# Kernel optimization log

Hardware: AMD Instinct MI355X
Metric: run time of the kernel (lower is better)

The kernel has to match this reference:

```python
import jax, jax.numpy as jnp
import numpy as np

B, S, E, H, L, FF = 32, 256, 768, 12, 2, 2048
DH = E // H
N_HIST, N_TGT = 128, 127  # fixed layout: pos0=type0, 1..128=type1 (hist), 129..255=type2 (target)
HIST_MASK_RATIO, MASK_RATIO, TAU = 0.5, 0.5, 1.0
KEEP_HIST = max(1, int(N_HIST * (1.0 - HIST_MASK_RATIO)))  # 64
KEEP_TGT = max(1, int(N_TGT * (1.0 - MASK_RATIO)))        # 63
INFERENCE = False
EPS = 1e-5
NEG = -1e30


def _sinusoidal_pe():
    pos = np.arange(257, dtype=np.float32)[:, None]
    div = np.exp(np.arange(0, E, 2, dtype=np.float32) * (-np.log(10000.0) / E))
    pe = np.zeros((257, E), np.float32)
    pe[:, 0::2] = np.sin(pos * div)
    pe[:, 1::2] = np.cos(pos * div)
    return jnp.asarray(pe)


def setup_inputs() -> dict:
    key = jax.random.key(0)
    ks = jax.random.split(key, 12)
    rn = lambda k, sh, s=1.0: jax.random.normal(k, sh, dtype=jnp.float32) * s
    inp = {}
    inp['token_embeds'] = rn(ks[0], (B, S, E))
    inp['attention_mask'] = jnp.zeros((B, S), dtype=bool)  # no padding
    inp['position_ids'] = jnp.tile(jnp.arange(S, dtype=jnp.int32), (B, 1))
    row = jnp.concatenate([jnp.zeros((1,), jnp.int32), jnp.ones((N_HIST,), jnp.int32), jnp.full((N_TGT,), 2, jnp.int32)])
    inp['type_ids'] = jnp.tile(row, (B, 1))
    inp['gumbel_hist'] = jax.random.gumbel(ks[1], (B, S), dtype=jnp.float32)
    inp['gumbel_target'] = jax.random.gumbel(ks[2], (B, S), dtype=jnp.float32)
    inp['pe'] = _sinusoidal_pe()
    inp['type_emb'] = rn(ks[3], (3, E), 0.02)
    inp['ln_w'] = jnp.ones((E,), jnp.float32); inp['ln_b'] = jnp.zeros((E,), jnp.float32)
    inp['dense_w'] = rn(ks[4], (E, E), 0.02); inp['dense_b'] = jnp.zeros((E,), jnp.float32)
    inp['qkv_w'] = rn(ks[5], (L, 3 * E, E), 0.02); inp['qkv_b'] = jnp.zeros((L, 3 * E), jnp.float32)
    inp['out_w'] = rn(ks[6], (L, E, E), 0.02); inp['out_b'] = jnp.zeros((L, E), jnp.float32)
    inp['ln1_w'] = jnp.ones((L, E), jnp.float32); inp['ln1_b'] = jnp.zeros((L, E), jnp.float32)
    inp['lin1_w'] = rn(ks[7], (L, FF, E), 0.02); inp['lin1_b'] = jnp.zeros((L, FF), jnp.float32)
    inp['lin2_w'] = rn(ks[8], (L, E, FF), 0.02); inp['lin2_b'] = jnp.zeros((L, E), jnp.float32)
    inp['ln2_w'] = jnp.ones((L, E), jnp.float32); inp['ln2_b'] = jnp.zeros((L, E), jnp.float32)
    return inp


def _ln(x, w, b):
    m = x.mean(-1, keepdims=True)
    v = jnp.mean((x - m) ** 2, -1, keepdims=True)
    return (x - m) * jax.lax.rsqrt(v + EPS) * w + b


def _masked_softmax(score, m):
    e = jnp.exp(score) * m
    return e / jnp.sum(e, -1, keepdims=True)


def _gumbel_topk(prob, valid, gumbel, keep_num):
    vm = valid.astype(prob.dtype)
    logits = jnp.where(valid, jnp.log(jnp.where(valid, prob, 1.0)), NEG)
    gl = jnp.where(valid, (logits + gumbel) / TAU, NEG)
    y_soft = jax.nn.softmax(gl, axis=-1)  # invalid positions get exactly 0
    idx = jax.lax.top_k(y_soft, keep_num)[1]
    y_hard = jnp.zeros_like(y_soft).at[jnp.arange(B)[:, None], idx].set(1.0)
    return (y_hard - jax.lax.stop_gradient(y_soft) + y_soft) * vm


def reference(token_embeds, attention_mask, position_ids, type_ids, gumbel_hist, gumbel_target,
              pe, type_emb, ln_w, ln_b, dense_w, dense_b, qkv_w, qkv_b, out_w, out_b,
              ln1_w, ln1_b, lin1_w, lin1_b, lin2_w, lin2_b, ln2_w, ln2_b):
    # get_input_embeds (dropout = identity in eval)
    x = _ln(token_embeds + pe[position_ids] + type_emb[type_ids], ln_w, ln_b)
    # TransformerEncoder (post-norm, relu FFN, key_padding_mask)
    kpm = attention_mask[:, None, None, :]
    for l in range(L):
        qkv = x @ qkv_w[l].T + qkv_b[l]
        q, k, v = jnp.split(qkv, 3, axis=-1)
        q = q.reshape(B, S, H, DH); k = k.reshape(B, S, H, DH); v = v.reshape(B, S, H, DH)
        sc = jnp.einsum('bqhd,bkhd->bhqk', q, k) / np.float32(np.sqrt(DH))
        sc = jnp.where(kpm, NEG, sc)
        o = jnp.einsum('bhqk,bkhd->bqhd', jax.nn.softmax(sc, -1), v).reshape(B, S, E)
        x = _ln(x + o @ out_w[l].T + out_b[l], ln1_w[l], ln1_b[l])
        f = jax.nn.relu(x @ lin1_w[l].T + lin1_b[l]) @ lin2_w[l].T + lin2_b[l]
        x = _ln(x + f, ln2_w[l], ln2_b[l])
    out = _ln(x, ln_w, ln_b)
    out = jnp.tanh(out @ dense_w.T + dense_b)
    # cosine similarity (torch eps=1e-8)
    na = jnp.linalg.norm(token_embeds, axis=-1)
    nb = jnp.linalg.norm(out, axis=-1)
    cos = jnp.sum(token_embeds * out, -1) / jnp.maximum(na * nb, 1e-8)
    hist_mask = type_ids == 1
    tgt_mask = type_ids == 2
    hp = _masked_softmax(cos, hist_mask.astype(cos.dtype))
    tp0 = _masked_softmax(cos, tgt_mask.astype(cos.dtype))
    tp = tp0 if INFERENCE else 1.0 - tp0
    hist_ret = _gumbel_topk(hp, hist_mask, gumbel_hist, KEEP_HIST)
    tgt_ret = _gumbel_topk(tp, tgt_mask, gumbel_target, KEEP_TGT)
    return hist_ret + tgt_ret
```

## Files before the change

kernel.cpp:

```cpp
#include <hip/hip_runtime.h>
#include <math.h>

#define B_ 32
#define S_ 256
#define E_ 768
#define H_ 12
#define L_ 2
#define FF_ 2048
#define NEGV -1e30f

typedef __attribute__((ext_vector_type(8))) short bf16x8;
typedef __attribute__((ext_vector_type(4))) float f32x4;

__device__ __forceinline__ short bf16_rne(float x) {
  unsigned u = __float_as_uint(x);
  u += 0x7fffu + ((u >> 16) & 1u);
  return (short)(u >> 16);
}
__device__ __forceinline__ float bf16_to_f32(short h) {
  return __uint_as_float(((unsigned)(unsigned short)h) << 16);
}
__device__ __forceinline__ void split_bf16(float v, short& h, short& l) {
  h = bf16_rne(v);
  l = bf16_rne(v - bf16_to_f32(h));
}

__device__ __forceinline__ void gl2lds16(const short* g, short* s) {
  __builtin_amdgcn_global_load_lds((const __attribute__((address_space(1))) void*)g,
                                   (__attribute__((address_space(3))) void*)s, 16, 0, 0);
}

__device__ __forceinline__ float block_sum256(float v) {
  __shared__ float sh[4];
  int lane = threadIdx.x & 63, w = threadIdx.x >> 6;
#pragma unroll
  for (int off = 32; off; off >>= 1) v += __shfl_down(v, off);
  if (lane == 0) sh[w] = v;
  __syncthreads();
  float tot = sh[0] + sh[1] + sh[2] + sh[3];
  __syncthreads();
  return tot;
}

__global__ __launch_bounds__(256) void embed_ln_kernel(
    const float* __restrict__ tok, const int* __restrict__ pos,
    const int* __restrict__ typ, const float* __restrict__ pe,
    const float* __restrict__ temb, const float* __restrict__ w,
    const float* __restrict__ b, float* __restrict__ out,
    short* __restrict__ ohi, short* __restrict__ olo) {
  int row = blockIdx.x;
  int t = threadIdx.x;
  int p = pos[row], ty = typ[row];
  const float* tr = tok + (size_t)row * E_;
  const float* pr = pe + (size_t)p * E_;
  const float* yr = temb + (size_t)ty * E_;
  float v0 = tr[t] + pr[t] + yr[t];
  float v1 = tr[t + 256] + pr[t + 256] + yr[t + 256];
  float v2 = tr[t + 512] + pr[t + 512] + yr[t + 512];
  float m = block_sum256(v0 + v1 + v2) * (1.f / E_);
  float d0 = v0 - m, d1 = v1 - m, d2 = v2 - m;
  float var = block_sum256(d0 * d0 + d1 * d1 + d2 * d2) * (1.f / E_);
  float rs = 1.f / sqrtf(var + 1e-5f);
  size_t base = (size_t)row * E_;
  float r0 = d0 * rs * w[t] + b[t];
  float r1 = d1 * rs * w[t + 256] + b[t + 256];
  float r2 = d2 * rs * w[t + 512] + b[t + 512];
  out[base + t] = r0; out[base + t + 256] = r1; out[base + t + 512] = r2;
  short h, l;
  split_bf16(r0, h, l); ohi[base + t] = h; olo[base + t] = l;
  split_bf16(r1, h, l); ohi[base + t + 256] = h; olo[base + t + 256] = l;
  split_bf16(r2, h, l); ohi[base + t + 512] = h; olo[base + t + 512] = l;
}

__global__ __launch_bounds__(256) void ln_kernel(
    const float* __restrict__ in, const float* __restrict__ w,
    const float* __restrict__ b, float* __restrict__ out,
    short* __restrict__ ohi, short* __restrict__ olo) {
  int row = blockIdx.x;
  int t = threadIdx.x;
  const float* p = in + (size_t)row * E_;
  float v0 = p[t], v1 = p[t + 256], v2 = p[t + 512];
  float m = block_sum256(v0 + v1 + v2) * (1.f / E_);
  float d0 = v0 - m, d1 = v1 - m, d2 = v2 - m;
  float var = block_sum256(d0 * d0 + d1 * d1 + d2 * d2) * (1.f / E_);
  float rs = 1.f / sqrtf(var + 1e-5f);
  size_t base = (size_t)row * E_;
  float r0 = d0 * rs * w[t] + b[t];
  float r1 = d1 * rs * w[t + 256] + b[t + 256];
  float r2 = d2 * rs * w[t + 512] + b[t + 512];
  if (out) {
    out[base + t] = r0; out[base + t + 256] = r1; out[base + t + 512] = r2;
  }
  short h, l;
  split_bf16(r0, h, l); ohi[base + t] = h; olo[base + t] = l;
  split_bf16(r1, h, l); ohi[base + t + 256] = h; olo[base + t + 256] = l;
  split_bf16(r2, h, l); ohi[base + t + 512] = h; olo[base + t + 512] = l;
}

__global__ __launch_bounds__(256) void split_kernel(
    const float* __restrict__ src, short* __restrict__ hi,
    short* __restrict__ lo, int n4) {
  int i = blockIdx.x * 256 + threadIdx.x;
  if (i >= n4) return;
  float4 v = ((const float4*)src)[i];
  short4 h, l;
  split_bf16(v.x, h.x, l.x);
  split_bf16(v.y, h.y, l.y);
  split_bf16(v.z, h.z, l.z);
  split_bf16(v.w, h.w, l.w);
  ((short4*)hi)[i] = h;
  ((short4*)lo)[i] = l;
}

template <int ACT, int RES, int OSPLIT>
__global__ __launch_bounds__(256, 2) void gemm_dp(
    const short* __restrict__ Ahi, const short* __restrict__ Alo,
    const short* __restrict__ Whi, const short* __restrict__ Wlo,
    const float* __restrict__ bias, const float* __restrict__ Rres,
    float* __restrict__ Cf, short* __restrict__ Chi, short* __restrict__ Clo,
    int M, int N, int K, int nx, int cpx) {
  __shared__ short lds[2 * 16384];
  const int t = threadIdx.x;
  const int l = t & 63;
  const int w = t >> 6;
  int id = blockIdx.x;
  int id2 = (id & 7) * cpx + (id >> 3);
  const int n0 = (id2 % nx) * 128, m0 = (id2 / nx) * 128;
  const int wm = (w >> 1) * 64, wn = (w & 1) * 64;

  const int g_kb = (l & 3) ^ ((l >> 3) & 3);
  const int r0 = w * 16 + (l >> 2);
  const int r1 = r0 + 64;
  const size_t aof0 = (size_t)(m0 + r0) * K + g_kb * 8;
  const size_t aof1 = (size_t)(m0 + r1) * K + g_kb * 8;
  const size_t wof0 = (size_t)(n0 + r0) * K + g_kb * 8;
  const size_t wof1 = (size_t)(n0 + r1) * K + g_kb * 8;
  const short* pAh0 = Ahi + aof0; const short* pAh1 = Ahi + aof1;
  const short* pAl0 = Alo + aof0; const short* pAl1 = Alo + aof1;
  const short* pWh0 = Whi + wof0; const short* pWh1 = Whi + wof1;
  const short* pWl0 = Wlo + wof0; const short* pWl1 = Wlo + wof1;

  const int kb_r = ((l >> 4) ^ ((l >> 1) & 3)) * 8;
  const short* ra = lds + (wm + (l & 15)) * 32 + kb_r;
  const short* rb = lds + (wn + (l & 15)) * 32 + kb_r;

  f32x4 acc[4][4] = {};
  const int ns = K >> 5;

  auto stage = [&](int buf, int k0) {
    short* base = lds + buf * 16384;
    gl2lds16(pAh0 + k0, base + w * 512);
    gl2lds16(pAh1 + k0, base + (4 + w) * 512);
    gl2lds16(pAl0 + k0, base + 4096 + w * 512);
    gl2lds16(pAl1 + k0, base + 4096 + (4 + w) * 512);
    gl2lds16(pWh0 + k0, base + 8192 + w * 512);
    gl2lds16(pWh1 + k0, base + 8192 + (4 + w) * 512);
    gl2lds16(pWl0 + k0, base + 12288 + w * 512);
    gl2lds16(pWl1 + k0, base + 12288 + (4 + w) * 512);
  };

  stage(0, 0);

  for (int s = 0; s < ns; ++s) {
    const int bp = s & 1;
    __builtin_amdgcn_s_barrier();
    if (s + 1 < ns) {
      stage(bp ^ 1, (s + 1) * 32);
      __builtin_amdgcn_sched_barrier(0);
      asm volatile("s_waitcnt vmcnt(8)" ::: "memory");
    } else {
      __builtin_amdgcn_sched_barrier(0);
      asm volatile("s_waitcnt vmcnt(0)" ::: "memory");
    }
    __builtin_amdgcn_s_barrier();

    const short* rab = ra + bp * 16384;
    const short* rbb = rb + bp * 16384;
    bf16x8 ah[4], al[4], bh[4], bl[4];
#pragma unroll
    for (int i = 0; i < 4; i++) {
      ah[i] = *(const bf16x8*)(rab + i * 512);
      al[i] = *(const bf16x8*)(rab + 4096 + i * 512);
      bh[i] = *(const bf16x8*)(rbb + 8192 + i * 512);
      bl[i] = *(const bf16x8*)(rbb + 12288 + i * 512);
    }
    __builtin_amdgcn_s_setprio(1);
#pragma unroll
    for (int mi = 0; mi < 4; mi++)
#pragma unroll
      for (int ni = 0; ni < 4; ni++) {
        acc[mi][ni] = __builtin_amdgcn_mfma_f32_16x16x32_bf16(ah[mi], bh[ni], acc[mi][ni], 0, 0, 0);
        acc[mi][ni] = __builtin_amdgcn_mfma_f32_16x16x32_bf16(ah[mi], bl[ni], acc[mi][ni], 0, 0, 0);
        acc[mi][ni] = __builtin_amdgcn_mfma_f32_16x16x32_bf16(al[mi], bh[ni], acc[mi][ni], 0, 0, 0);
      }
    __builtin_amdgcn_s_setprio(0);
  }

  const int col_l = l & 15;
  const int row_l = (l >> 4) * 4;
#pragma unroll
  for (int mi = 0; mi < 4; mi++) {
#pragma unroll
    for (int ni = 0; ni < 4; ni++) {
      int col = n0 + wn + ni * 16 + col_l;
      float bv = bias[col];
#pragma unroll
      for (int r = 0; r < 4; r++) {
        int row = m0 + wm + mi * 16 + row_l + r;
        float v = acc[mi][ni][r] + bv;
        if (RES) v += Rres[(size_t)row * N + col];
        if (ACT == 1) v = fmaxf(v, 0.f);
        if (ACT == 2) v = tanhf(v);
        if (OSPLIT) {
          short h2, l2;
          split_bf16(v, h2, l2);
          Chi[(size_t)row * N + col] = h2;
          Clo[(size_t)row * N + col] = l2;
        } else {
          Cf[(size_t)row * N + col] = v;
        }
      }
    }
  }
}

template <int ACT, int RES>
__global__ __launch_bounds__(256, 2) void gemm_dp2(
    const short* __restrict__ Ahi, const short* __restrict__ Alo,
    const short* __restrict__ Whi, const short* __restrict__ Wlo,
    const float* __restrict__ bias, const float* __restrict__ Rres,
    float* __restrict__ Cf, int M, int N, int K, int nx, int cpx) {
  __shared__ short lds[2 * 20480];
  const int t = threadIdx.x;
  const int l = t & 63;
  const int w = t >> 6;
  int id = blockIdx.x;
  int id2 = (id & 7) * cpx + (id >> 3);
  const int n0 = (id2 % nx) * 192, m0 = (id2 / nx) * 128;
  const int wm = (w >> 1) * 64;
  const int wn = (w & 1) * 96;

  const int g_kb = (l & 3) ^ ((l >> 3) & 3);
  const int srow = w * 16 + (l >> 2);
  const size_t a0 = (size_t)(m0 + srow) * K + g_kb * 8;
  const size_t a1 = (size_t)(m0 + 64 + srow) * K + g_kb * 8;
  const size_t w0 = (size_t)(n0 + srow) * K + g_kb * 8;
  const size_t w1 = (size_t)(n0 + 64 + srow) * K + g_kb * 8;
  const size_t w2 = (size_t)(n0 + 128 + srow) * K + g_kb * 8;
  const short* pAh0 = Ahi + a0; const short* pAh1 = Ahi + a1;
  const short* pAl0 = Alo + a0; const short* pAl1 = Alo + a1;
  const short* pWh0 = Whi + w0; const short* pWh1 = Whi + w1; const short* pWh2 = Whi + w2;
  const short* pWl0 = Wlo + w0; const short* pWl1 = Wlo + w1; const short* pWl2 = Wlo + w2;

  const int kb_r = ((l >> 4) ^ ((l >> 1) & 3)) * 8;
  const short* ra = lds + (wm + (l & 15)) * 32 + kb_r;
  const short* rb = lds + 8192 + (wn + (l & 15)) * 32 + kb_r;

  f32x4 acc[4][6] = {};
  const int ns = K >> 5;

  auto stage = [&](int buf, int k0) {
    short* base = lds + buf * 20480;
    gl2lds16(pAh0 + k0, base + w * 512);
    gl2lds16(pAh1 + k0, base + 2048 + w * 512);
    gl2lds16(pAl0 + k0, base + 4096 + w * 512);
    gl2lds16(pAl1 + k0, base + 4096 + 2048 + w * 512);
    gl2lds16(pWh0 + k0, base + 8192 + w * 512);
    gl2lds16(pWh1 + k0, base + 8192 + 2048 + w * 512);
    gl2lds16(pWh2 + k0, base + 8192 + 4096 + w * 512);
    gl2lds16(pWl0 + k0, base + 14336 + w * 512);
    gl2lds16(pWl1 + k0, base + 14336 + 2048 + w * 512);
    gl2lds16(pWl2 + k0, base + 14336 + 4096 + w * 512);
  };

  stage(0, 0);

  for (int s = 0; s < ns; ++s) {
    const int bp = s & 1;
    __builtin_amdgcn_s_barrier();
    if (s + 1 < ns) {
      stage(bp ^ 1, (s + 1) * 32);
      __builtin_amdgcn_sched_barrier(0);
      asm volatile("s_waitcnt vmcnt(10)" ::: "memory");
    } else {
      __builtin_amdgcn_sched_barrier(0);
      asm volatile("s_waitcnt vmcnt(0)" ::: "memory");
    }
    __builtin_amdgcn_s_barrier();

    const short* rab = ra + bp * 20480;
    const short* rbb = rb + bp * 20480;
    bf16x8 bh[6], bl[6];
#pragma unroll
    for (int i = 0; i < 6; i++) {
      bh[i] = *(const bf16x8*)(rbb + i * 512);
      bl[i] = *(const bf16x8*)(rbb + 6144 + i * 512);
    }
    __builtin_amdgcn_s_setprio(1);
#pragma unroll
    for (int mi = 0; mi < 4; mi++) {
      bf16x8 ah = *(const bf16x8*)(rab + mi * 512);
      bf16x8 al = *(const bf16x8*)(rab + 4096 + mi * 512);
#pragma unroll
      for (int ni = 0; ni < 6; ni++) {
        acc[mi][ni] = __builtin_amdgcn_mfma_f32_16x16x32_bf16(ah, bh[ni], acc[mi][ni], 0, 0, 0);
        acc[mi][ni] = __builtin_amdgcn_mfma_f32_16x16x32_bf16(ah, bl[ni], acc[mi][ni], 0, 0, 0);
        acc[mi][ni] = __builtin_amdgcn_mfma_f32_16x16x32_bf16(al, bh[ni], acc[mi][ni], 0, 0, 0);
      }
    }
    __builtin_amdgcn_s_setprio(0);
  }

  const int col_l = l & 15;
  const int row_l = (l >> 4) * 4;
#pragma unroll
  for (int mi = 0; mi < 4; mi++) {
#pragma unroll
    for (int ni = 0; ni < 6; ni++) {
      int col = n0 + wn + ni * 16 + col_l;
      float bv = bias[col];
#pragma unroll
      for (int r = 0; r < 4; r++) {
        int row = m0 + wm + mi * 16 + row_l + r;
        float v = acc[mi][ni][r] + bv;
        if (RES) v += Rres[(size_t)row * N + col];
        if (ACT == 2) v = tanhf(v);
        Cf[(size_t)row * N + col] = v;
      }
    }
  }
}

__global__ __launch_bounds__(256, 2) void attn_kernel(
    const float* __restrict__ qkv, short* __restrict__ t1h,
    short* __restrict__ t1l) {
  __shared__ short lds[16384];
  const int qt = blockIdx.x, h = blockIdx.y, b = blockIdx.z;
  const int t = threadIdx.x;
  const int w = t >> 6, l = t & 63;
  const int li = l & 15, lh = l >> 4;

  short* kh = lds;
  short* kl = lds + 4096;
  short* ph = lds + 8192 + w * 2048;
  short* pl = ph + 1024;

  const int tok0 = b * S_ + qt * 64;

  bf16x8 qh[2], ql[2];
  {
    const float* qrow = qkv + (size_t)(tok0 + w * 16 + li) * 2304 + h * 64 + lh * 8;
#pragma unroll
    for (int s = 0; s < 2; s++) {
      float4 f0 = *(const float4*)(qrow + s * 32);
      float4 f1 = *(const float4*)(qrow + s * 32 + 4);
      float f[8] = {f0.x, f0.y, f0.z, f0.w, f1.x, f1.y, f1.z, f1.w};
      bf16x8 hv, lv;
#pragma unroll
      for (int j = 0; j < 8; j++) {
        short hs, ls2;
        split_bf16(f[j], hs, ls2);
        hv[j] = hs; lv[j] = ls2;
      }
      qh[s] = hv; ql[s] = lv;
    }
  }

  const int skk = t >> 2, sd0 = (t & 3) * 16;

  f32x4 acc[16] = {};

  const float* kbase = qkv + (size_t)(b * S_) * 2304 + 768 + h * 64;
#pragma unroll
  for (int c = 0; c < 4; c++) {
    __syncthreads();
    {
      const float* src = kbase + (size_t)(c * 64 + skk) * 2304 + sd0;
#pragma unroll
      for (int i = 0; i < 4; i++) {
        float4 f = *(const float4*)(src + i * 4);
        int d = sd0 + i * 4;
        short4 hv, lv;
        split_bf16(f.x, hv.x, lv.x);
        split_bf16(f.y, hv.y, lv.y);
        split_bf16(f.z, hv.z, lv.z);
        split_bf16(f.w, hv.w, lv.w);
        int off = skk * 64 + ((((d >> 3) ^ (skk & 7)) & 7) << 3) + (d & 7);
        *(short4*)(kh + off) = hv;
        *(short4*)(kl + off) = lv;
      }
    }
    __syncthreads();
#pragma unroll
    for (int nn = 0; nn < 4; nn++) {
      const int krow = nn * 16 + li;
#pragma unroll
      for (int s = 0; s < 2; s++) {
        const int off = krow * 64 + ((((s * 4 + lh) ^ (li & 7)) & 7) << 3);
        bf16x8 bh = *(const bf16x8*)(kh + off);
        bf16x8 bl = *(const bf16x8*)(kl + off);
        acc[c * 4 + nn] = __builtin_amdgcn_mfma_f32_16x16x32_bf16(qh[s], bh, acc[c * 4 + nn], 0, 0, 0);
        acc[c * 4 + nn] = __builtin_amdgcn_mfma_f32_16x16x32_bf16(qh[s], bl, acc[c * 4 + nn], 0, 0, 0);
        acc[c * 4 + nn] = __builtin_amdgcn_mfma_f32_16x16x32_bf16(ql[s], bh, acc[c * 4 + nn], 0, 0, 0);
      }
    }
  }

  float rs_[4];
#pragma unroll
  for (int r = 0; r < 4; r++) {
    float m = -3.4e38f;
#pragma unroll
    for (int fi = 0; fi < 16; fi++) m = fmaxf(m, acc[fi][r]);
#pragma unroll
    for (int off = 8; off; off >>= 1) m = fmaxf(m, __shfl_xor(m, off));
    float sum = 0.f;
#pragma unroll
    for (int fi = 0; fi < 16; fi++) {
      float p = expf((acc[fi][r] - m) * 0.125f);
      acc[fi][r] = p;
      sum += p;
    }
#pragma unroll
    for (int off = 8; off; off >>= 1) sum += __shfl_xor(sum, off);
    rs_[r] = sum;
  }

  f32x4 oacc[4] = {};
  const float* vbase = qkv + (size_t)(b * S_) * 2304 + 1536 + h * 64;
#pragma unroll
  for (int c = 0; c < 4; c++) {
    __syncthreads();
    {
      const float* src = vbase + (size_t)(c * 64 + skk) * 2304 + sd0;
#pragma unroll
      for (int i = 0; i < 4; i++) {
        float4 f = *(const float4*)(src + i * 4);
        float fv[4] = {f.x, f.y, f.z, f.w};
#pragma unroll
        for (int j = 0; j < 4; j++) {
          int d = sd0 + i * 4 + j;
          short hs, ls2;
          split_bf16(fv[j], hs, ls2);
          int sw = (d & 7) ^ ((d >> 3) & 7);
          int off = d * 64 + ((((skk >> 3) ^ sw) & 7) << 3) + (skk & 7);
          kh[off] = hs;
          kl[off] = ls2;
        }
      }
    }
#pragma unroll
    for (int nn = 0; nn < 4; nn++) {
#pragma unroll
      for (int r = 0; r < 4; r++) {
        const int q = lh * 4 + r;
        const int keyl = li + 16 * nn;
        short hs, ls2;
        split_bf16(acc[c * 4 + nn][r], hs, ls2);
        const int off = q * 64 + ((((keyl >> 3) ^ (q & 7)) & 7) << 3) + (keyl & 7);
        ph[off] = hs;
        pl[off] = ls2;
      }
    }
    __syncthreads();
    bf16x8 pah[2], pal[2];
#pragma unroll
    for (int s = 0; s < 2; s++) {
      const int off = li * 64 + ((((s * 4 + lh) ^ (li & 7)) & 7) << 3);
      pah[s] = *(const bf16x8*)(ph + off);
      pal[s] = *(const bf16x8*)(pl + off);
    }
#pragma unroll
    for (int dn = 0; dn < 4; dn++) {
      const int drow = dn * 16 + li;
      const int sw = ((drow & 7) ^ ((drow >> 3) & 7)) & 7;
#pragma unroll
      for (int s = 0; s < 2; s++) {
        const int off = drow * 64 + ((((s * 4 + lh) ^ sw) & 7) << 3);
        bf16x8 vh = *(const bf16x8*)(kh + off);
        bf16x8 vl = *(const bf16x8*)(kl + off);
        oacc[dn] = __builtin_amdgcn_mfma_f32_16x16x32_bf16(pah[s], vh, oacc[dn], 0, 0, 0);
        oacc[dn] = __builtin_amdgcn_mfma_f32_16x16x32_bf16(pah[s], vl, oacc[dn], 0, 0, 0);
        oacc[dn] = __builtin_amdgcn_mfma_f32_16x16x32_bf16(pal[s], vh, oacc[dn], 0, 0, 0);
      }
    }
  }

  float rinv[4];
#pragma unroll
  for (int r = 0; r < 4; r++) rinv[r] = 1.f / rs_[r];
#pragma unroll
  for (int dn = 0; dn < 4; dn++) {
#pragma unroll
    for (int r = 0; r < 4; r++) {
      float v = oacc[dn][r] * rinv[r];
      short hs, ls2;
      split_bf16(v, hs, ls2);
      size_t oidx = (size_t)(tok0 + w * 16 + lh * 4 + r) * E_ + h * 64 + dn * 16 + li;
      t1h[oidx] = hs;
      t1l[oidx] = ls2;
    }
  }
}

__global__ __launch_bounds__(256) void cos_kernel(
    const float* __restrict__ a, const float* __restrict__ o,
    float* __restrict__ cosv) {
  int row = blockIdx.x;
  int t = threadIdx.x;
  const float* ar = a + (size_t)row * E_;
  const float* orr = o + (size_t)row * E_;
  float d = 0.f, na = 0.f, nb = 0.f;
#pragma unroll
  for (int j = 0; j < 3; j++) {
    float av = ar[t + 256 * j], ov = orr[t + 256 * j];
    d = fmaf(av, ov, d);
    na = fmaf(av, av, na);
    nb = fmaf(ov, ov, nb);
  }
  d = block_sum256(d);
  na = block_sum256(na);
  nb = block_sum256(nb);
  if (t == 0) cosv[row] = d / fmaxf(sqrtf(na) * sqrtf(nb), 1e-8f);
}

__global__ __launch_bounds__(256) void select_kernel(
    const float* __restrict__ cosv, const int* __restrict__ typ,
    const float* __restrict__ gh, const float* __restrict__ gt,
    float* __restrict__ out) {
  __shared__ float vals[256];
  int b = blockIdx.x, t = threadIdx.x;
  int idx = b * 256 + t;
  int ty = typ[idx];
  float c = cosv[idx];
  float res = 0.f;

  float eh = (ty == 1) ? expf(c) : 0.f;
  float sh = block_sum256(eh);
  float glh = (ty == 1) ? (logf(eh / sh) + gh[idx]) : NEGV;
  vals[t] = glh;
  __syncthreads();
  {
    int rank = 0;
#pragma unroll
    for (int j = 0; j < 64; ++j) {
      float4 q = *(const float4*)&vals[j * 4];
      rank += (q.x > glh) || (q.x == glh && (j * 4 + 0) < t);
      rank += (q.y > glh) || (q.y == glh && (j * 4 + 1) < t);
      rank += (q.z > glh) || (q.z == glh && (j * 4 + 2) < t);
      rank += (q.w > glh) || (q.w == glh && (j * 4 + 3) < t);
    }
    if (ty == 1 && rank < 64) res += 1.f;
  }
  __syncthreads();

  float et = (ty == 2) ? expf(c) : 0.f;
  float st = block_sum256(et);
  float glt = (ty == 2) ? (logf(1.f - et / st) + gt[idx]) : NEGV;
  vals[t] = glt;
  __syncthreads();
  {
    int rank = 0;
#pragma unroll
    for (int j = 0; j < 64; ++j) {
      float4 q = *(const float4*)&vals[j * 4];
      rank += (q.x > glt) || (q.x == glt && (j * 4 + 0) < t);
      rank += (q.y > glt) || (q.y == glt && (j * 4 + 1) < t);
      rank += (q.z > glt) || (q.z == glt && (j * 4 + 2) < t);
      rank += (q.w > glt) || (q.w == glt && (j * 4 + 3) < t);
    }
    if (ty == 2 && rank < 63) res += 1.f;
  }
  out[idx] = res;
}

static void launch_gemm(int act, int res, int osplit, const short* Ahi,
                        const short* Alo, const short* Whi, const short* Wlo,
                        const float* bias, const float* R, float* Cf,
                        short* Chi, short* Clo, int M, int N, int K,
                        hipStream_t s) {
  int nx = N / 128, ny = M / 128;
  int nwg = nx * ny;
  int cpx = nwg / 8;
  dim3 grid(nwg), blk(256);
  if (osplit) {
    gemm_dp<1, 0, 1><<<grid, blk, 0, s>>>(Ahi, Alo, Whi, Wlo, bias, R, Cf, Chi, Clo, M, N, K, nx, cpx);
  } else if (act == 2) {
    gemm_dp<2, 0, 0><<<grid, blk, 0, s>>>(Ahi, Alo, Whi, Wlo, bias, R, Cf, Chi, Clo, M, N, K, nx, cpx);
  } else if (res) {
    gemm_dp<0, 1, 0><<<grid, blk, 0, s>>>(Ahi, Alo, Whi, Wlo, bias, R, Cf, Chi, Clo, M, N, K, nx, cpx);
  } else {
    gemm_dp<0, 0, 0><<<grid, blk, 0, s>>>(Ahi, Alo, Whi, Wlo, bias, R, Cf, Chi, Clo, M, N, K, nx, cpx);
  }
}

static void launch_gemm2(int act, int res, const short* Ahi, const short* Alo,
                         const short* Whi, const short* Wlo, const float* bias,
                         const float* R, float* Cf, int M, int N, int K,
                         hipStream_t s) {
  int nx = N / 192, ny = M / 128;
  int nwg = nx * ny;
  int cpx = nwg / 8;
  dim3 grid(nwg), blk(256);
  if (act == 2) {
    gemm_dp2<2, 0><<<grid, blk, 0, s>>>(Ahi, Alo, Whi, Wlo, bias, R, Cf, M, N, K, nx, cpx);
  } else if (res) {
    gemm_dp2<0, 1><<<grid, blk, 0, s>>>(Ahi, Alo, Whi, Wlo, bias, R, Cf, M, N, K, nx, cpx);
  } else {
    gemm_dp2<0, 0><<<grid, blk, 0, s>>>(Ahi, Alo, Whi, Wlo, bias, R, Cf, M, N, K, nx, cpx);
  }
}

extern "C" void kernel_launch(void* const* d_in, const int* in_sizes, int n_in,
                              void* d_out, int out_size, void* d_ws,
                              size_t ws_size, hipStream_t stream) {
  const float* tok = (const float*)d_in[0];
  const int* pos = (const int*)d_in[2];
  const int* typ = (const int*)d_in[3];
  const float* gh = (const float*)d_in[4];
  const float* gt = (const float*)d_in[5];
  const float* pe = (const float*)d_in[6];
  const float* temb = (const float*)d_in[7];
  const float* ln_w = (const float*)d_in[8];
  const float* ln_b = (const float*)d_in[9];
  const float* dense_w = (const float*)d_in[10];
  const float* dense_b = (const float*)d_in[11];
  const float* qkv_w = (const float*)d_in[12];
  const float* qkv_b = (const float*)d_in[13];
  const float* out_w = (const float*)d_in[14];
  const float* out_b = (const float*)d_in[15];
  const float* ln1_w = (const float*)d_in[16];
  const float* ln1_b = (const float*)d_in[17];
  const float* lin1_w = (const float*)d_in[18];
  const float* lin1_b = (const float*)d_in[19];
  const float* lin2_w = (const float*)d_in[20];
  const float* lin2_b = (const float*)d_in[21];
  const float* ln2_w = (const float*)d_in[22];
  const float* ln2_b = (const float*)d_in[23];

  const int M = B_ * S_;
  const size_t NX = (size_t)M * E_;
  const size_t NQKV = (size_t)M * 3 * E_;
  const size_t NFF = (size_t)M * FF_;

  const size_t oQ = 0;
  const size_t oO = oQ + 2 * (size_t)3 * E_ * E_;
  const size_t oL1 = oO + 2 * (size_t)E_ * E_;
  const size_t oL2 = oL1 + 2 * (size_t)FF_ * E_;
  const size_t oD = oL2 + 2 * (size_t)E_ * FF_;
  const size_t WTOT = oD + (size_t)E_ * E_;

  float* ws = (float*)d_ws;
  float* x = ws;
  float* t2 = x + NX;
  float* shared = t2 + NX;
  short* x_hi = (short*)(shared + NQKV);
  short* x_lo = x_hi + NX;
  short* t1_hi = x_lo + NX;
  short* t1_lo = t1_hi + NX;
  short* w_hi = t1_lo + NX;
  short* w_lo = w_hi + WTOT;
  float* cosb = (float*)(w_lo + WTOT);

  short* big_hi = (short*)shared;
  short* big_lo = big_hi + NFF;

  {
    int n4;
    n4 = (int)(2 * 3 * E_ * E_ / 4);
    split_kernel<<<(n4 + 255) / 256, 256, 0, stream>>>(qkv_w, w_hi + oQ, w_lo + oQ, n4);
    n4 = (int)(2 * E_ * E_ / 4);
    split_kernel<<<(n4 + 255) / 256, 256, 0, stream>>>(out_w, w_hi + oO, w_lo + oO, n4);
    n4 = (int)(2 * FF_ * E_ / 4);
    split_kernel<<<(n4 + 255) / 256, 256, 0, stream>>>(lin1_w, w_hi + oL1, w_lo + oL1, n4);
    n4 = (int)(2 * E_ * FF_ / 4);
    split_kernel<<<(n4 + 255) / 256, 256, 0, stream>>>(lin2_w, w_hi + oL2, w_lo + oL2, n4);
    n4 = (int)(E_ * E_ / 4);
    split_kernel<<<(n4 + 255) / 256, 256, 0, stream>>>(dense_w, w_hi + oD, w_lo + oD, n4);
  }

  embed_ln_kernel<<<M, 256, 0, stream>>>(tok, pos, typ, pe, temb, ln_w, ln_b,
                                         x, x_hi, x_lo);

  for (int l = 0; l < L_; l++) {
    const size_t wq = oQ + (size_t)l * 3 * E_ * E_;
    const size_t wo = oO + (size_t)l * E_ * E_;
    const size_t w1 = oL1 + (size_t)l * FF_ * E_;
    const size_t w2 = oL2 + (size_t)l * E_ * FF_;
    launch_gemm2(0, 0, x_hi, x_lo, w_hi + wq, w_lo + wq,
                 qkv_b + (size_t)l * 3 * E_, nullptr, shared, M, 3 * E_, E_,
                 stream);
    attn_kernel<<<dim3(4, H_, B_), 256, 0, stream>>>(shared, t1_hi, t1_lo);
    launch_gemm2(0, 1, t1_hi, t1_lo, w_hi + wo, w_lo + wo,
                 out_b + (size_t)l * E_, x, t2, M, E_, E_, stream);
    ln_kernel<<<M, 256, 0, stream>>>(t2, ln1_w + (size_t)l * E_,
                                     ln1_b + (size_t)l * E_, x, x_hi, x_lo);
    launch_gemm(1, 0, 1, x_hi, x_lo, w_hi + w1, w_lo + w1,
                lin1_b + (size_t)l * FF_, nullptr, nullptr, big_hi, big_lo,
                M, FF_, E_, stream);
    launch_gemm2(0, 1, big_hi, big_lo, w_hi + w2, w_lo + w2,
                 lin2_b + (size_t)l * E_, x, t2, M, E_, FF_, stream);
    ln_kernel<<<M, 256, 0, stream>>>(t2, ln2_w + (size_t)l * E_,
                                     ln2_b + (size_t)l * E_, x, x_hi, x_lo);
  }

  ln_kernel<<<M, 256, 0, stream>>>(x, ln_w, ln_b, nullptr, t1_hi, t1_lo);
  launch_gemm2(2, 0, t1_hi, t1_lo, w_hi + oD, w_lo + oD, dense_b, nullptr,
               shared, M, E_, E_, stream);
  cos_kernel<<<M, 256, 0, stream>>>(tok, shared, cosb);
  select_kernel<<<B_, 256, 0, stream>>>(cosb, typ, gh, gt, (float*)d_out);
}
```

Before: 836.7 us.

## Emit split bf16 QKV from GEMM epilogue and load it directly in attention

The QKV projection GEMM now writes hi/lo bf16 halves instead of fp32, and the attention kernel reads those halves directly. Q is loaded as vectors and K is staged into LDS with direct global-to-LDS copies, using a source-side swizzle. This removes the per-element fp32 split work that attention repeated for every query tile and keeps total QKV traffic the same size. The risk is that the GEMM epilogue now does more scalar short stores, and the gl2lds path adds a wait on outstanding memory loads.

Result: no change. 844.0 us (+0.9%).

```diff
diff --git a/kernel.cpp b/kernel.cpp
--- a/kernel.cpp
+++ b/kernel.cpp
@@ -224,12 +224,13 @@
   }
 }
 
-template <int ACT, int RES>
+template <int ACT, int RES, int OSPLIT>
 __global__ __launch_bounds__(256, 2) void gemm_dp2(
     const short* __restrict__ Ahi, const short* __restrict__ Alo,
     const short* __restrict__ Whi, const short* __restrict__ Wlo,
     const float* __restrict__ bias, const float* __restrict__ Rres,
-    float* __restrict__ Cf, int M, int N, int K, int nx, int cpx) {
+    float* __restrict__ Cf, short* __restrict__ Chi, short* __restrict__ Clo,
+    int M, int N, int K, int nx, int cpx) {
   __shared__ short lds[2 * 20480];
   const int t = threadIdx.x;
   const int l = t & 63;
@@ -325,15 +326,22 @@
         float v = acc[mi][ni][r] + bv;
         if (RES) v += Rres[(size_t)row * N + col];
         if (ACT == 2) v = tanhf(v);
-        Cf[(size_t)row * N + col] = v;
+        if (OSPLIT) {
+          short h2, l2;
+          split_bf16(v, h2, l2);
+          Chi[(size_t)row * N + col] = h2;
+          Clo[(size_t)row * N + col] = l2;
+        } else {
+          Cf[(size_t)row * N + col] = v;
+        }
       }
     }
   }
 }
 
 __global__ __launch_bounds__(256, 2) void attn_kernel(
-    const float* __restrict__ qkv, short* __restrict__ t1h,
-    short* __restrict__ t1l) {
+    const short* __restrict__ qkvh, const short* __restrict__ qkvl,
+    short* __restrict__ t1h, short* __restrict__ t1l) {
   __shared__ short lds[16384];
   const int qt = blockIdx.x, h = blockIdx.y, b = blockIdx.z;
   const int t = threadIdx.x;
@@ -349,47 +357,30 @@
 
   bf16x8 qh[2], ql[2];
   {
-    const float* qrow = qkv + (size_t)(tok0 + w * 16 + li) * 2304 + h * 64 + lh * 8;
+    const size_t qoff = (size_t)(tok0 + w * 16 + li) * 2304 + h * 64 + lh * 8;
 #pragma unroll
     for (int s = 0; s < 2; s++) {
-      float4 f0 = *(const float4*)(qrow + s * 32);
-      float4 f1 = *(const float4*)(qrow + s * 32 + 4);
-      float f[8] = {f0.x, f0.y, f0.z, f0.w, f1.x, f1.y, f1.z, f1.w};
-      bf16x8 hv, lv;
-#pragma unroll
-      for (int j = 0; j < 8; j++) {
-        short hs, ls2;
-        split_bf16(f[j], hs, ls2);
-        hv[j] = hs; lv[j] = ls2;
-      }
-      qh[s] = hv; ql[s] = lv;
+      qh[s] = *(const bf16x8*)(qkvh + qoff + s * 32);
+      ql[s] = *(const bf16x8*)(qkvl + qoff + s * 32);
     }
   }
 
   const int skk = t >> 2, sd0 = (t & 3) * 16;
+  const int src_db = (l & 7) ^ ((l >> 3) & 7);
 
   f32x4 acc[16] = {};
 
-  const float* kbase = qkv + (size_t)(b * S_) * 2304 + 768 + h * 64;
 #pragma unroll
   for (int c = 0; c < 4; c++) {
     __syncthreads();
-    {
-      const float* src = kbase + (size_t)(c * 64 + skk) * 2304 + sd0;
-#pragma unroll
-      for (int i = 0; i < 4; i++) {
-        float4 f = *(const float4*)(src + i * 4);
-        int d = sd0 + i * 4;
-        short4 hv, lv;
-        split_bf16(f.x, hv.x, lv.x);
-        split_bf16(f.y, hv.y, lv.y);
-        split_bf16(f.z, hv.z, lv.z);
-        split_bf16(f.w, hv.w, lv.w);
-        int off = skk * 64 + ((((d >> 3) ^ (skk & 7)) & 7) << 3) + (d & 7);
-        *(short4*)(kh + off) = hv;
-        *(short4*)(kl + off) = lv;
-      }
-    }
+#pragma unroll
+    for (int j = 0; j < 2; j++) {
+      int r = c * 64 + w * 16 + j * 8 + (l >> 3);
+      const size_t so = (size_t)(b * S_ + r) * 2304 + 768 + h * 64 + src_db * 8;
+      gl2lds16(qkvh + so, kh + (w * 2 + j) * 512);
+      gl2lds16(qkvl + so, kl + (w * 2 + j) * 512);
+    }
+    asm volatile("s_waitcnt vmcnt(0)" ::: "memory");
     __syncthreads();
 #pragma unroll
     for (int nn = 0; nn < 4; nn++) {
@@ -427,26 +418,24 @@
   }
 
   f32x4 oacc[4] = {};
-  const float* vbase = qkv + (size_t)(b * S_) * 2304 + 1536 + h * 64;
 #pragma unroll
   for (int c = 0; c < 4; c++) {
     __syncthreads();
     {
-      const float* src = vbase + (size_t)(c * 64 + skk) * 2304 + sd0;
-#pragma unroll
-      for (int i = 0; i < 4; i++) {
-        float4 f = *(const float4*)(src + i * 4);
-        float fv[4] = {f.x, f.y, f.z, f.w};
-#pragma unroll
-        for (int j = 0; j < 4; j++) {
-          int d = sd0 + i * 4 + j;
-          short hs, ls2;
-          split_bf16(fv[j], hs, ls2);
-          int sw = (d & 7) ^ ((d >> 3) & 7);
-          int off = d * 64 + ((((skk >> 3) ^ sw) & 7) << 3) + (skk & 7);
-          kh[off] = hs;
-          kl[off] = ls2;
-        }
+      const size_t so = (size_t)(b * S_ + c * 64 + skk) * 2304 + 1536 + h * 64 + sd0;
+      bf16x8 hv0 = *(const bf16x8*)(qkvh + so);
+      bf16x8 hv1 = *(const bf16x8*)(qkvh + so + 8);
+      bf16x8 lv0 = *(const bf16x8*)(qkvl + so);
+      bf16x8 lv1 = *(const bf16x8*)(qkvl + so + 8);
+#pragma unroll
+      for (int j = 0; j < 16; j++) {
+        int d = sd0 + j;
+        short hs = (j < 8) ? hv0[j & 7] : hv1[j & 7];
+        short ls2 = (j < 8) ? lv0[j & 7] : lv1[j & 7];
+        int sw = (d & 7) ^ ((d >> 3) & 7);
+        int off = d * 64 + ((((skk >> 3) ^ sw) & 7) << 3) + (skk & 7);
+        kh[off] = hs;
+        kl[off] = ls2;
       }
     }
 #pragma unroll
@@ -594,20 +583,23 @@
   }
 }
 
-static void launch_gemm2(int act, int res, const short* Ahi, const short* Alo,
-                         const short* Whi, const short* Wlo, const float* bias,
-                         const float* R, float* Cf, int M, int N, int K,
+static void launch_gemm2(int act, int res, int osplit, const short* Ahi,
+                         const short* Alo, const short* Whi, const short* Wlo,
+                         const float* bias, const float* R, float* Cf,
+                         short* Chi, short* Clo, int M, int N, int K,
                          hipStream_t s) {
   int nx = N / 192, ny = M / 128;
   int nwg = nx * ny;
   int cpx = nwg / 8;
   dim3 grid(nwg), blk(256);
-  if (act == 2) {
-    gemm_dp2<2, 0><<<grid, blk, 0, s>>>(Ahi, Alo, Whi, Wlo, bias, R, Cf, M, N, K, nx, cpx);
+  if (osplit) {
+    gemm_dp2<0, 0, 1><<<grid, blk, 0, s>>>(Ahi, Alo, Whi, Wlo, bias, R, Cf, Chi, Clo, M, N, K, nx, cpx);
+  } else if (act == 2) {
+    gemm_dp2<2, 0, 0><<<grid, blk, 0, s>>>(Ahi, Alo, Whi, Wlo, bias, R, Cf, Chi, Clo, M, N, K, nx, cpx);
   } else if (res) {
-    gemm_dp2<0, 1><<<grid, blk, 0, s>>>(Ahi, Alo, Whi, Wlo, bias, R, Cf, M, N, K, nx, cpx);
+    gemm_dp2<0, 1, 0><<<grid, blk, 0, s>>>(Ahi, Alo, Whi, Wlo, bias, R, Cf, Chi, Clo, M, N, K, nx, cpx);
   } else {
-    gemm_dp2<0, 0><<<grid, blk, 0, s>>>(Ahi, Alo, Whi, Wlo, bias, R, Cf, M, N, K, nx, cpx);
+    gemm_dp2<0, 0, 0><<<grid, blk, 0, s>>>(Ahi, Alo, Whi, Wlo, bias, R, Cf, Chi, Clo, M, N, K, nx, cpx);
   }
 }
 
@@ -662,6 +654,8 @@
   short* w_lo = w_hi + WTOT;
   float* cosb = (float*)(w_lo + WTOT);
 
+  short* qkv_hi = (short*)shared;
+  short* qkv_lo = qkv_hi + NQKV;
   short* big_hi = (short*)shared;
   short* big_lo = big_hi + NFF;
 
@@ -687,26 +681,26 @@
     const size_t wo = oO + (size_t)l * E_ * E_;
     const size_t w1 = oL1 + (size_t)l * FF_ * E_;
     const size_t w2 = oL2 + (size_t)l * E_ * FF_;
-    launch_gemm2(0, 0, x_hi, x_lo, w_hi + wq, w_lo + wq,
-                 qkv_b + (size_t)l * 3 * E_, nullptr, shared, M, 3 * E_, E_,
-                 stream);
-    attn_kernel<<<dim3(4, H_, B_), 256, 0, stream>>>(shared, t1_hi, t1_lo);
-    launch_gemm2(0, 1, t1_hi, t1_lo, w_hi + wo, w_lo + wo,
-                 out_b + (size_t)l * E_, x, t2, M, E_, E_, stream);
+    launch_gemm2(0, 0, 1, x_hi, x_lo, w_hi + wq, w_lo + wq,
+                 qkv_b + (size_t)l * 3 * E_, nullptr, nullptr, qkv_hi, qkv_lo,
+                 M, 3 * E_, E_, stream);
+    attn_kernel<<<dim3(4, H_, B_), 256, 0, stream>>>(qkv_hi, qkv_lo, t1_hi, t1_lo);
+    launch_gemm2(0, 1, 0, t1_hi, t1_lo, w_hi + wo, w_lo + wo,
+                 out_b + (size_t)l * E_, x, t2, nullptr, nullptr, M, E_, E_, stream);
     ln_kernel<<<M, 256, 0, stream>>>(t2, ln1_w + (size_t)l * E_,
                                      ln1_b + (size_t)l * E_, x, x_hi, x_lo);
     launch_gemm(1, 0, 1, x_hi, x_lo, w_hi + w1, w_lo + w1,
                 lin1_b + (size_t)l * FF_, nullptr, nullptr, big_hi, big_lo,
                 M, FF_, E_, stream);
-    launch_gemm2(0, 1, big_hi, big_lo, w_hi + w2, w_lo + w2,
-                 lin2_b + (size_t)l * E_, x, t2, M, E_, FF_, stream);
+    launch_gemm2(0, 1, 0, big_hi, big_lo, w_hi + w2, w_lo + w2,
+                 lin2_b + (size_t)l * E_, x, t2, nullptr, nullptr, M, E_, FF_, stream);
     ln_kernel<<<M, 256, 0, stream>>>(t2, ln2_w + (size_t)l * E_,
                                      ln2_b + (size_t)l * E_, x, x_hi, x_lo);
   }
 
   ln_kernel<<<M, 256, 0, stream>>>(x, ln_w, ln_b, nullptr, t1_hi, t1_lo);
-  launch_gemm2(2, 0, t1_hi, t1_lo, w_hi + oD, w_lo + oD, dense_b, nullptr,
-               shared, M, E_, E_, stream);
+  launch_gemm2(2, 0, 0, t1_hi, t1_lo, w_hi + oD, w_lo + oD, dense_b, nullptr,
+               shared, nullptr, nullptr, M, E_, E_, stream);
   cos_kernel<<<M, 256, 0, stream>>>(tok, shared, cosb);
   select_kernel<<<B_, 256, 0, stream>>>(cosb, typ, gh, gt, (float*)d_out);
 }
```

## Use 256-row, 512-thread GEMM tiles for QKV and FFN1 projections

Applied to the files above, without the earlier changes.

Replaces the 128x128 GEMM used for FFN1, and the 128x192 GEMM used for QKV, with a templated 512-thread kernel using 256-row tiles (256x288 for QKV, 256x256 for FFN1). Each launch becomes exactly 256 workgroups, which should fill the GPU in one wave and raise operand reuse per LDS load. The kernel also loads B fragments per column inside the inner loop and preloads bias. The cost is larger LDS use and higher register pressure per block. The QKV config leaves a remainder of load chunks that only half the threads fetch, which needs per-wave waitcnt handling.

New measurement: 815.0 us. 2.6% less time.

```diff
diff --git a/kernel.cpp b/kernel.cpp
--- a/kernel.cpp
+++ b/kernel.cpp
@@ -112,52 +112,65 @@
   ((short4*)lo)[i] = l;
 }
 
-template <int ACT, int RES, int OSPLIT>
-__global__ __launch_bounds__(256, 2) void gemm_dp(
+template <int BN_, int WM_, int WN_, int ACT, int OSPLIT>
+__global__ __launch_bounds__(512, 2) void gemm_big(
     const short* __restrict__ Ahi, const short* __restrict__ Alo,
     const short* __restrict__ Whi, const short* __restrict__ Wlo,
-    const float* __restrict__ bias, const float* __restrict__ Rres,
-    float* __restrict__ Cf, short* __restrict__ Chi, short* __restrict__ Clo,
+    const float* __restrict__ bias, float* __restrict__ Cf,
+    short* __restrict__ Chi, short* __restrict__ Clo,
     int M, int N, int K, int nx, int cpx) {
-  __shared__ short lds[2 * 16384];
+  constexpr int BM_ = 256;
+  constexpr int MR = WM_ / 16, NR = WN_ / 16;
+  constexpr int NWC = BN_ / WN_;
+  constexpr int CHUNKS = 2 * BM_ + 2 * BN_;
+  constexpr int OPS_FULL = CHUNKS / 128;
+  constexpr int REM = CHUNKS - OPS_FULL * 128;
+  constexpr int BUFSH = CHUNKS * 32;
+
+  __shared__ short lds[2 * BUFSH];
   const int t = threadIdx.x;
   const int l = t & 63;
   const int w = t >> 6;
+  const int wr = w / NWC, wc = w % NWC;
+  const int li = l & 15, lh = l >> 4;
+
   int id = blockIdx.x;
   int id2 = (id & 7) * cpx + (id >> 3);
-  const int n0 = (id2 % nx) * 128, m0 = (id2 / nx) * 128;
-  const int wm = (w >> 1) * 64, wn = (w & 1) * 64;
-
-  const int g_kb = (l & 3) ^ ((l >> 3) & 3);
-  const int r0 = w * 16 + (l >> 2);
-  const int r1 = r0 + 64;
-  const size_t aof0 = (size_t)(m0 + r0) * K + g_kb * 8;
-  const size_t aof1 = (size_t)(m0 + r1) * K + g_kb * 8;
-  const size_t wof0 = (size_t)(n0 + r0) * K + g_kb * 8;
-  const size_t wof1 = (size_t)(n0 + r1) * K + g_kb * 8;
-  const short* pAh0 = Ahi + aof0; const short* pAh1 = Ahi + aof1;
-  const short* pAl0 = Alo + aof0; const short* pAl1 = Alo + aof1;
-  const short* pWh0 = Whi + wof0; const short* pWh1 = Whi + wof1;
-  const short* pWl0 = Wlo + wof0; const short* pWl1 = Wlo + wof1;
-
-  const int kb_r = ((l >> 4) ^ ((l >> 1) & 3)) * 8;
-  const short* ra = lds + (wm + (l & 15)) * 32 + kb_r;
-  const short* rb = lds + (wn + (l & 15)) * 32 + kb_r;
-
-  f32x4 acc[4][4] = {};
+  const int n0 = (id2 % nx) * BN_, m0 = (id2 / nx) * BM_;
+
+  const int cks = t & 3;
+  auto mksrc = [&](int c) -> const short* {
+    const short* base; int row;
+    if (c < BM_) { base = Ahi; row = m0 + c; }
+    else if (c < 2 * BM_) { base = Alo; row = m0 + c - BM_; }
+    else if (c < 2 * BM_ + BN_) { base = Whi; row = n0 + c - 2 * BM_; }
+    else { base = Wlo; row = n0 + c - 2 * BM_ - BN_; }
+    return base + (size_t)row * K + (cks ^ ((c >> 1) & 3)) * 8;
+  };
+  const short* sp[OPS_FULL + 1];
+#pragma unroll
+  for (int o = 0; o < OPS_FULL; ++o) sp[o] = mksrc(o * 128 + (t >> 2));
+  if (REM) sp[OPS_FULL] = mksrc((t < 256) ? (OPS_FULL * 128 + (t >> 2)) : 0);
+
+  auto stage = [&](int buf, int k0) {
+    short* base = lds + buf * BUFSH;
+#pragma unroll
+    for (int o = 0; o < OPS_FULL; ++o)
+      gl2lds16(sp[o] + k0, base + o * 4096 + w * 512);
+    if (REM) {
+      if (t < 256)
+        gl2lds16(sp[OPS_FULL] + k0, base + OPS_FULL * 4096 + w * 512);
+    }
+  };
+
+  const int kb_r = (lh ^ ((l >> 1) & 3)) * 8;
+
+  float bv[NR];
+#pragma unroll
+  for (int ni = 0; ni < NR; ++ni) bv[ni] = bias[n0 + wc * WN_ + ni * 16 + li];
+
+  f32x4 acc[MR][NR] = {};
   const int ns = K >> 5;
-
-  auto stage = [&](int buf, int k0) {
-    short* base = lds + buf * 16384;
-    gl2lds16(pAh0 + k0, base + w * 512);
-    gl2lds16(pAh1 + k0, base + (4 + w) * 512);
-    gl2lds16(pAl0 + k0, base + 4096 + w * 512);
-    gl2lds16(pAl1 + k0, base + 4096 + (4 + w) * 512);
-    gl2lds16(pWh0 + k0, base + 8192 + w * 512);
-    gl2lds16(pWh1 + k0, base + 8192 + (4 + w) * 512);
-    gl2lds16(pWl0 + k0, base + 12288 + w * 512);
-    gl2lds16(pWl1 + k0, base + 12288 + (4 + w) * 512);
-  };
 
   stage(0, 0);
 
@@ -167,48 +180,56 @@
     if (s + 1 < ns) {
       stage(bp ^ 1, (s + 1) * 32);
       __builtin_amdgcn_sched_barrier(0);
-      asm volatile("s_waitcnt vmcnt(8)" ::: "memory");
+      if (REM) {
+        if (w < 4)
+          asm volatile("s_waitcnt vmcnt(%0)" ::"n"(OPS_FULL + 1) : "memory");
+        else
+          asm volatile("s_waitcnt vmcnt(%0)" ::"n"(OPS_FULL) : "memory");
+      } else {
+        asm volatile("s_waitcnt vmcnt(%0)" ::"n"(OPS_FULL) : "memory");
+      }
     } else {
       __builtin_amdgcn_sched_barrier(0);
       asm volatile("s_waitcnt vmcnt(0)" ::: "memory");
     }
     __builtin_amdgcn_s_barrier();
 
-    const short* rab = ra + bp * 16384;
-    const short* rbb = rb + bp * 16384;
-    bf16x8 ah[4], al[4], bh[4], bl[4];
-#pragma unroll
-    for (int i = 0; i < 4; i++) {
-      ah[i] = *(const bf16x8*)(rab + i * 512);
-      al[i] = *(const bf16x8*)(rab + 4096 + i * 512);
-      bh[i] = *(const bf16x8*)(rbb + 8192 + i * 512);
-      bl[i] = *(const bf16x8*)(rbb + 12288 + i * 512);
+    const short* bufp = lds + bp * BUFSH;
+    bf16x8 ah[MR], al[MR];
+#pragma unroll
+    for (int mi = 0; mi < MR; ++mi) {
+      int row = wr * WM_ + mi * 16 + li;
+      ah[mi] = *(const bf16x8*)(bufp + row * 32 + kb_r);
+      al[mi] = *(const bf16x8*)(bufp + BM_ * 32 + row * 32 + kb_r);
     }
     __builtin_amdgcn_s_setprio(1);
 #pragma unroll
-    for (int mi = 0; mi < 4; mi++)
-#pragma unroll
-      for (int ni = 0; ni < 4; ni++) {
-        acc[mi][ni] = __builtin_amdgcn_mfma_f32_16x16x32_bf16(ah[mi], bh[ni], acc[mi][ni], 0, 0, 0);
-        acc[mi][ni] = __builtin_amdgcn_mfma_f32_16x16x32_bf16(ah[mi], bl[ni], acc[mi][ni], 0, 0, 0);
-        acc[mi][ni] = __builtin_amdgcn_mfma_f32_16x16x32_bf16(al[mi], bh[ni], acc[mi][ni], 0, 0, 0);
-      }
+    for (int ni = 0; ni < NR; ++ni) {
+      int rowB = wc * WN_ + ni * 16 + li;
+      bf16x8 bh = *(const bf16x8*)(bufp + 2 * BM_ * 32 + rowB * 32 + kb_r);
+      bf16x8 bl = *(const bf16x8*)(bufp + (2 * BM_ + BN_) * 32 + rowB * 32 + kb_r);
+#pragma unroll
+      for (int mi = 0; mi < MR; ++mi) {
+        acc[mi][ni] = __builtin_amdgcn_mfma_f32_16x16x32_bf16(ah[mi], bh, acc[mi][ni], 0, 0, 0);
+        acc[mi][ni] = __builtin_amdgcn_mfma_f32_16x16x32_bf16(ah[mi], bl, acc[mi][ni], 0, 0, 0);
+        acc[mi][ni] = __builtin_amdgcn_mfma_f32_16x16x32_bf16(al[mi], bh, acc[mi][ni], 0, 0, 0);
+      }
+    }
     __builtin_amdgcn_s_setprio(0);
   }
 
   const int col_l = l & 15;
   const int row_l = (l >> 4) * 4;
 #pragma unroll
-  for (int mi = 0; mi < 4; mi++) {
-#pragma unroll
-    for (int ni = 0; ni < 4; ni++) {
-      int col = n0 + wn + ni * 16 + col_l;
-      float bv = bias[col];
-#pragma unroll
-      for (int r = 0; r < 4; r++) {
-        int row = m0 + wm + mi * 16 + row_l + r;
-        float v = acc[mi][ni][r] + bv;
-        if (RES) v += Rres[(size_t)row * N + col];
+  for (int mi = 0; mi < MR; ++mi) {
+#pragma unroll
+    for (int ni = 0; ni < NR; ++ni) {
+      int col = n0 + wc * WN_ + ni * 16 + col_l;
+      float bvv = bv[ni];
+#pragma unroll
+      for (int r = 0; r < 4; ++r) {
+        int row = m0 + wr * WM_ + mi * 16 + row_l + r;
+        float v = acc[mi][ni][r] + bvv;
         if (ACT == 1) v = fmaxf(v, 0.f);
         if (ACT == 2) v = tanhf(v);
         if (OSPLIT) {
@@ -572,26 +593,6 @@
     if (ty == 2 && rank < 63) res += 1.f;
   }
   out[idx] = res;
-}
-
-static void launch_gemm(int act, int res, int osplit, const short* Ahi,
-                        const short* Alo, const short* Whi, const short* Wlo,
-                        const float* bias, const float* R, float* Cf,
-                        short* Chi, short* Clo, int M, int N, int K,
-                        hipStream_t s) {
-  int nx = N / 128, ny = M / 128;
-  int nwg = nx * ny;
-  int cpx = nwg / 8;
-  dim3 grid(nwg), blk(256);
-  if (osplit) {
-    gemm_dp<1, 0, 1><<<grid, blk, 0, s>>>(Ahi, Alo, Whi, Wlo, bias, R, Cf, Chi, Clo, M, N, K, nx, cpx);
-  } else if (act == 2) {
-    gemm_dp<2, 0, 0><<<grid, blk, 0, s>>>(Ahi, Alo, Whi, Wlo, bias, R, Cf, Chi, Clo, M, N, K, nx, cpx);
-  } else if (res) {
-    gemm_dp<0, 1, 0><<<grid, blk, 0, s>>>(Ahi, Alo, Whi, Wlo, bias, R, Cf, Chi, Clo, M, N, K, nx, cpx);
-  } else {
-    gemm_dp<0, 0, 0><<<grid, blk, 0, s>>>(Ahi, Alo, Whi, Wlo, bias, R, Cf, Chi, Clo, M, N, K, nx, cpx);
-  }
 }
 
 static void launch_gemm2(int act, int res, const short* Ahi, const short* Alo,
@@ -687,17 +688,17 @@
     const size_t wo = oO + (size_t)l * E_ * E_;
     const size_t w1 = oL1 + (size_t)l * FF_ * E_;
     const size_t w2 = oL2 + (size_t)l * E_ * FF_;
-    launch_gemm2(0, 0, x_hi, x_lo, w_hi + wq, w_lo + wq,
-                 qkv_b + (size_t)l * 3 * E_, nullptr, shared, M, 3 * E_, E_,
-                 stream);
+    gemm_big<288, 64, 144, 0, 0><<<256, 512, 0, stream>>>(
+        x_hi, x_lo, w_hi + wq, w_lo + wq, qkv_b + (size_t)l * 3 * E_, shared,
+        nullptr, nullptr, M, 3 * E_, E_, 3 * E_ / 288, 32);
     attn_kernel<<<dim3(4, H_, B_), 256, 0, stream>>>(shared, t1_hi, t1_lo);
     launch_gemm2(0, 1, t1_hi, t1_lo, w_hi + wo, w_lo + wo,
                  out_b + (size_t)l * E_, x, t2, M, E_, E_, stream);
     ln_kernel<<<M, 256, 0, stream>>>(t2, ln1_w + (size_t)l * E_,
                                      ln1_b + (size_t)l * E_, x, x_hi, x_lo);
-    launch_gemm(1, 0, 1, x_hi, x_lo, w_hi + w1, w_lo + w1,
-                lin1_b + (size_t)l * FF_, nullptr, nullptr, big_hi, big_lo,
-                M, FF_, E_, stream);
+    gemm_big<256, 128, 64, 1, 1><<<256, 512, 0, stream>>>(
+        x_hi, x_lo, w_hi + w1, w_lo + w1, lin1_b + (size_t)l * FF_, nullptr,
+        big_hi, big_lo, M, FF_, E_, FF_ / 256, 32);
     launch_gemm2(0, 1, big_hi, big_lo, w_hi + w2, w_lo + w2,
                  lin2_b + (size_t)l * E_, x, t2, M, E_, FF_, stream);
     ln_kernel<<<M, 256, 0, stream>>>(t2, ln2_w + (size_t)l * E_,
```
